# Kernel optimization log

Measured on AMD Instinct MI355X. Metric: run time of the kernel, lower is better.

The kernel has to match this reference:

```python
import jax, jax.numpy as jnp
import numpy as np

B, T, H, K = 128, 512, 1024, 7
START, STOP = 5, 6
NEG = -10000.0


def setup_inputs() -> dict:
    key = jax.random.key(0)
    k1, k2, k3, k4, k5, k6 = jax.random.split(key, 6)
    features = jax.random.normal(k1, (B, T, H), dtype=jnp.float32)
    tags = jax.random.randint(k2, (B, T), 0, 5, dtype=jnp.int32)  # BIESO only
    lengths = jax.random.randint(k3, (B,), 1, T + 1, dtype=jnp.int32)
    W = jax.random.normal(k4, (K, H), dtype=jnp.float32) * (1.0 / np.sqrt(H))
    b = jax.random.normal(k5, (K,), dtype=jnp.float32) * 0.01
    transitions = jax.random.normal(k6, (K, K), dtype=jnp.float32)
    transitions = transitions.at[START, :].set(NEG)  # nothing transitions into START
    transitions = transitions.at[:, STOP].set(NEG)   # nothing transitions out of STOP
    return {"features": features, "tags": tags, "lengths": lengths,
            "W": W, "b": b, "transitions": transitions}


def _crf_loss(features, W, b, transitions, tags, lengths):
    feats = jnp.einsum('bth,kh->btk', features, W) + b  # [B,T,K] emissions
    Bn, Tn, Kn = feats.shape

    # ---- forward algorithm (partition function) ----
    init = jnp.full((Bn, Kn), NEG, dtype=feats.dtype).at[:, START].set(0.0)

    def step(fv, inp):
        emit, i = inp  # emit: [B,K]
        # tag_var[b, next, prev] = emit[b, next] + trans[next, prev] + fv[b, prev]
        tv = emit[:, :, None] + transitions[None, :, :] + fv[:, None, :]
        new = jax.nn.logsumexp(tv, axis=2)  # [B,K]
        fv = jnp.where((i < lengths)[:, None], new, fv)  # freeze past sentence end
        return fv, None

    fv, _ = jax.lax.scan(step, init, (jnp.swapaxes(feats, 0, 1), jnp.arange(Tn)))
    terminal = fv + transitions[STOP][None, :]
    forward_score = jax.nn.logsumexp(terminal, axis=1)  # [B]

    # ---- gold score ----
    pad_start = jnp.concatenate(
        [jnp.full((Bn, 1), START, tags.dtype), tags], axis=1)  # [B,T+1]
    pad_stop = jnp.concatenate(
        [tags, jnp.full((Bn, 1), STOP, tags.dtype)], axis=1)   # [B,T+1]
    j = jnp.arange(Tn + 1)[None, :]
    pad_stop = jnp.where(j >= lengths[:, None], STOP, pad_stop)
    trans_sc = jnp.sum(
        jnp.where(j <= lengths[:, None], transitions[pad_stop, pad_start], 0.0),
        axis=1)
    t = jnp.arange(Tn)[None, :]
    emit_sel = jnp.take_along_axis(feats, tags[:, :, None].astype(jnp.int32), axis=2)[:, :, 0]
    emit_sc = jnp.sum(jnp.where(t < lengths[:, None], emit_sel, 0.0), axis=1)
    gold_score = trans_sc + emit_sc  # [B]

    return jnp.sum(forward_score - gold_score)


def reference(features, tags, lengths, W, b, transitions):
    return _crf_loss(features, W, b, transitions, tags, lengths)
```

## Files before the change

kernel.cpp:

```cpp
#include <hip/hip_runtime.h>

#define B_ 128
#define T_ 512
#define H_ 1024
#define K_ 7
#define START_ 5
#define STOP_ 6
#define LOG2E 1.4426950408889634f
#define LN2 0.6931471805599453f
#define NEG2 (-10000.0f * 1.4426950408889634f)
#define MS 57

__device__ __forceinline__ float fexp2(float x) { return __builtin_amdgcn_exp2f(x); }
__device__ __forceinline__ float flog2(float x) { return __builtin_amdgcn_logf(x); }

__global__ __launch_bounds__(256, 2) void emis_kernel(
    const float* __restrict__ features, const float* __restrict__ W,
    const float* __restrict__ bias, float* __restrict__ e2, float* __restrict__ out) {
  if (blockIdx.x == 0 && threadIdx.x == 0) out[0] = 0.0f;

  const int tid = threadIdx.x;
  const int lane = tid & 63;
  const int gwave = blockIdx.x * 4 + (tid >> 6);
  const int NW = 8192;

  float4 w[K_][4];
#pragma unroll
  for (int k = 0; k < K_; ++k)
#pragma unroll
    for (int c = 0; c < 4; ++c)
      w[k][c] = *(const float4*)(W + k * H_ + c * 256 + lane * 4);

  const int vidx = ((lane & 1) << 2) | (lane & 2) | ((lane >> 2) & 1);
  float myb = 0.0f;
  if (vidx < K_) myb = bias[vidx];

  float4 A0, A1, A2, A3, B0, B1, B2, B3;
  {
    const float4* fp = (const float4*)(features + (size_t)gwave * H_);
    A0 = fp[lane]; A1 = fp[64 + lane]; A2 = fp[128 + lane]; A3 = fp[192 + lane];
    const float4* gp = (const float4*)(features + (size_t)(gwave + NW) * H_);
    B0 = gp[lane]; B1 = gp[64 + lane]; B2 = gp[128 + lane]; B3 = gp[192 + lane];
  }

#pragma unroll
  for (int it = 0; it < 8; ++it) {
    const int cur = gwave + it * NW;
    float4 C0, C1, C2, C3;
    if (it < 6) {
      const float4* pp = (const float4*)(features + (size_t)(cur + 2 * NW) * H_);
      C0 = pp[lane]; C1 = pp[64 + lane]; C2 = pp[128 + lane]; C3 = pp[192 + lane];
    }

    float acc[8];
#pragma unroll
    for (int k = 0; k < 8; ++k) acc[k] = 0.0f;
#pragma unroll
    for (int k = 0; k < K_; ++k) {
      acc[k] += A0.x * w[k][0].x + A0.y * w[k][0].y + A0.z * w[k][0].z + A0.w * w[k][0].w;
      acc[k] += A1.x * w[k][1].x + A1.y * w[k][1].y + A1.z * w[k][1].z + A1.w * w[k][1].w;
      acc[k] += A2.x * w[k][2].x + A2.y * w[k][2].y + A2.z * w[k][2].z + A2.w * w[k][2].w;
      acc[k] += A3.x * w[k][3].x + A3.y * w[k][3].y + A3.z * w[k][3].z + A3.w * w[k][3].w;
    }

    const bool b0 = lane & 1;
    float k0 = b0 ? acc[4] : acc[0], s0 = b0 ? acc[0] : acc[4];
    float k1 = b0 ? acc[5] : acc[1], s1 = b0 ? acc[1] : acc[5];
    float k2 = b0 ? acc[6] : acc[2], s2 = b0 ? acc[2] : acc[6];
    float k3 = b0 ? acc[7] : acc[3], s3 = b0 ? acc[3] : acc[7];
    k0 += __shfl_xor(s0, 1, 64); k1 += __shfl_xor(s1, 1, 64);
    k2 += __shfl_xor(s2, 1, 64); k3 += __shfl_xor(s3, 1, 64);
    const bool b1 = lane & 2;
    float m0 = b1 ? k2 : k0, t0 = b1 ? k0 : k2;
    float m1 = b1 ? k3 : k1, t1 = b1 ? k1 : k3;
    m0 += __shfl_xor(t0, 2, 64); m1 += __shfl_xor(t1, 2, 64);
    const bool b2 = lane & 4;
    float x = b2 ? m1 : m0, y = b2 ? m0 : m1;
    x += __shfl_xor(y, 4, 64);
    x += __shfl_xor(x, 8, 64);
    x += __shfl_xor(x, 16, 64);
    x += __shfl_xor(x, 32, 64);

    if (lane < 8 && vidx < K_)
      e2[(size_t)cur * 8 + vidx] = (x + myb) * LOG2E;

    A0 = B0; A1 = B1; A2 = B2; A3 = B3;
    if (it < 6) { B0 = C0; B1 = C1; B2 = C2; B3 = C3; }
  }
}

template <int NM>
__device__ __forceinline__ void level_fn(const float* __restrict__ evenB,
                                         const float* __restrict__ oddB,
                                         int qstride, float* __restrict__ dst,
                                         int tid) {
  constexpr int TOT = NM * 49;
  constexpr int NI = (TOT + 255) / 256;
  float tmp[NI];
#pragma unroll
  for (int i = 0; i < NI; ++i) {
    const int u = tid + i * 256;
    if (u < TOT) {
      const int q = u / 49, r = u - 49 * q, n = r / 7, p = r - 7 * n;
      const float* hi = oddB + q * qstride;
      const float* lo = evenB + q * qstride;
      float qq[7];
#pragma unroll
      for (int m = 0; m < 7; ++m) qq[m] = hi[n * 8 + m] + lo[m * 8 + p];
      float mx = fmaxf(fmaxf(fmaxf(qq[0], qq[1]), fmaxf(qq[2], qq[3])),
                       fmaxf(fmaxf(qq[4], qq[5]), qq[6]));
      float s = 0.f;
#pragma unroll
      for (int m = 0; m < 7; ++m) s += fexp2(qq[m] - mx);
      tmp[i] = mx + flog2(s);
    }
  }
  __syncthreads();
#pragma unroll
  for (int i = 0; i < NI; ++i) {
    const int u = tid + i * 256;
    if (u < TOT) {
      const int q = u / 49, r = u - 49 * q, n = r / 7, p = r - 7 * n;
      dst[q * MS + n * 8 + p] = tmp[i];
    }
  }
  __syncthreads();
}

__global__ __launch_bounds__(256) void scan_kernel(
    const float* __restrict__ e2, const int* __restrict__ tags,
    const int* __restrict__ lengths, const float* __restrict__ transitions,
    float* __restrict__ out) {
  __shared__ float s0[128 * MS];
  __shared__ float s1[128 * MS];
  __shared__ float tr2s[49];
  __shared__ float red[4];

  const int tid = threadIdx.x;
  const int b = blockIdx.x;
  const int len = lengths[b];

  if (tid < 49) tr2s[tid] = transitions[tid] * LOG2E;
  __syncthreads();

  const int* tg = tags + (size_t)b * T_;
  const float* ep = e2 + (size_t)b * T_ * 8;
  float gp = 0.f;
  for (int t = tid; t < len; t += 256) {
    const int tag = tg[t];
    const int prev = t ? tg[t - 1] : START_;
    gp += ep[(size_t)t * 8 + tag] + tr2s[tag * 7 + prev];
  }
#pragma unroll
  for (int off = 32; off; off >>= 1) gp += __shfl_xor(gp, off, 64);
  if ((tid & 63) == 0) red[tid >> 6] = gp;

  {
    const int t0 = 2 * tid, t1 = 2 * tid + 1;
    float P[7][7];
    if (t1 < len) {
      const float* e0p = ep + (size_t)t0 * 8;
      float c[7], e1[7];
#pragma unroll
      for (int m = 0; m < 7; ++m) c[m] = e0p[m];
#pragma unroll
      for (int n = 0; n < 7; ++n) e1[n] = e0p[8 + n];
#pragma unroll
      for (int n = 0; n < 7; ++n) {
        float a[7];
#pragma unroll
        for (int m = 0; m < 7; ++m) a[m] = tr2s[n * 7 + m] + c[m];
#pragma unroll
        for (int p = 0; p < 7; ++p) {
          float q[7];
#pragma unroll
          for (int m = 0; m < 7; ++m) q[m] = a[m] + tr2s[m * 7 + p];
          float mx = fmaxf(fmaxf(fmaxf(q[0], q[1]), fmaxf(q[2], q[3])),
                           fmaxf(fmaxf(q[4], q[5]), q[6]));
          float s = 0.f;
#pragma unroll
          for (int m = 0; m < 7; ++m) s += fexp2(q[m] - mx);
          P[n][p] = e1[n] + mx + flog2(s);
        }
      }
    } else if (t0 < len) {
      const float* e0p = ep + (size_t)t0 * 8;
#pragma unroll
      for (int n = 0; n < 7; ++n) {
        const float e0n = e0p[n];
#pragma unroll
        for (int p = 0; p < 7; ++p) P[n][p] = e0n + tr2s[n * 7 + p];
      }
    } else {
#pragma unroll
      for (int n = 0; n < 7; ++n)
#pragma unroll
        for (int p = 0; p < 7; ++p) P[n][p] = (n == p) ? 0.f : NEG2;
    }
    float* dstm = ((tid & 1) ? s1 : s0) + (tid >> 1) * MS;
#pragma unroll
    for (int n = 0; n < 7; ++n)
#pragma unroll
      for (int p = 0; p < 7; ++p) dstm[n * 8 + p] = P[n][p];
  }
  __syncthreads();

  level_fn<128>(s0, s1, MS, s0, tid);
  level_fn<64>(s0, s0 + MS, 2 * MS, s1, tid);
  level_fn<32>(s1, s1 + MS, 2 * MS, s0, tid);
  level_fn<16>(s0, s0 + MS, 2 * MS, s1, tid);
  level_fn<8>(s1, s1 + MS, 2 * MS, s0, tid);
  level_fn<4>(s0, s0 + MS, 2 * MS, s1, tid);
  level_fn<2>(s1, s1 + MS, 2 * MS, s0, tid);
  level_fn<1>(s0, s0 + MS, 2 * MS, s1, tid);

  if (tid == 0) {
    float tt[7];
#pragma unroll
    for (int n = 0; n < 7; ++n) tt[n] = s1[n * 8 + START_] + tr2s[STOP_ * 7 + n];
    float mx = tt[0];
#pragma unroll
    for (int n = 1; n < 7; ++n) mx = fmaxf(mx, tt[n]);
    float s = 0.f;
#pragma unroll
    for (int n = 0; n < 7; ++n) s += fexp2(tt[n] - mx);
    const float fwd = mx + flog2(s);
    const float gold = red[0] + red[1] + red[2] + red[3] +
                       tr2s[STOP_ * 7 + tg[len - 1]];
    atomicAdd(out, (fwd - gold) * LN2);
  }
}

extern "C" void kernel_launch(void* const* d_in, const int* in_sizes, int n_in,
                              void* d_out, int out_size, void* d_ws, size_t ws_size,
                              hipStream_t stream) {
  const float* features    = (const float*)d_in[0];
  const int*   tags        = (const int*)d_in[1];
  const int*   lengths     = (const int*)d_in[2];
  const float* W           = (const float*)d_in[3];
  const float* bias        = (const float*)d_in[4];
  const float* transitions = (const float*)d_in[5];
  float* out = (float*)d_out;
  float* e2  = (float*)d_ws;

  emis_kernel<<<2048, 256, 0, stream>>>(features, W, bias, e2, out);
  scan_kernel<<<B_, 256, 0, stream>>>(e2, tags, lengths, transitions, out);
}
```

Baseline: 63.87 us.

## Deepen emission prefetch with nontemporal loads; widen scan block and drop max-shift

The emission kernel now keeps three rows in flight instead of two and reads features through nontemporal loads, aiming to hide more HBM latency on the streaming 256MB read. The scan kernel moves to 512 threads: half build the pairwise transfer matrices while the other half compute the gold score in parallel, and the tree-reduction levels spread over more threads. The leaf logsumexp drops its max subtraction and adds a tiny epsilon, trading numerical safety for fewer ops. The extra live registers in the emission kernel could lower occupancy, and skipping the max can underflow when all terms are very negative, since transitions contain -10000 entries.

```diff
diff --git a/kernel.cpp b/kernel.cpp
--- a/kernel.cpp
+++ b/kernel.cpp
@@ -11,8 +11,13 @@
 #define NEG2 (-10000.0f * 1.4426950408889634f)
 #define MS 57
 
+typedef float f32x4 __attribute__((ext_vector_type(4)));
+
 __device__ __forceinline__ float fexp2(float x) { return __builtin_amdgcn_exp2f(x); }
 __device__ __forceinline__ float flog2(float x) { return __builtin_amdgcn_logf(x); }
+__device__ __forceinline__ f32x4 ntload(const float* p) {
+  return __builtin_nontemporal_load((const f32x4*)p);
+}
 
 __global__ __launch_bounds__(256, 2) void emis_kernel(
     const float* __restrict__ features, const float* __restrict__ W,
@@ -24,32 +29,34 @@
   const int gwave = blockIdx.x * 4 + (tid >> 6);
   const int NW = 8192;
 
-  float4 w[K_][4];
+  f32x4 w[K_][4];
 #pragma unroll
   for (int k = 0; k < K_; ++k)
 #pragma unroll
     for (int c = 0; c < 4; ++c)
-      w[k][c] = *(const float4*)(W + k * H_ + c * 256 + lane * 4);
+      w[k][c] = *(const f32x4*)(W + k * H_ + c * 256 + lane * 4);
 
   const int vidx = ((lane & 1) << 2) | (lane & 2) | ((lane >> 2) & 1);
   float myb = 0.0f;
   if (vidx < K_) myb = bias[vidx];
 
-  float4 A0, A1, A2, A3, B0, B1, B2, B3;
+  f32x4 A0, A1, A2, A3, B0, B1, B2, B3, C0, C1, C2, C3;
   {
-    const float4* fp = (const float4*)(features + (size_t)gwave * H_);
-    A0 = fp[lane]; A1 = fp[64 + lane]; A2 = fp[128 + lane]; A3 = fp[192 + lane];
-    const float4* gp = (const float4*)(features + (size_t)(gwave + NW) * H_);
-    B0 = gp[lane]; B1 = gp[64 + lane]; B2 = gp[128 + lane]; B3 = gp[192 + lane];
+    const float* fp = features + (size_t)gwave * H_ + lane * 4;
+    A0 = ntload(fp); A1 = ntload(fp + 256); A2 = ntload(fp + 512); A3 = ntload(fp + 768);
+    const float* gp = fp + (size_t)NW * H_;
+    B0 = ntload(gp); B1 = ntload(gp + 256); B2 = ntload(gp + 512); B3 = ntload(gp + 768);
+    const float* hp = gp + (size_t)NW * H_;
+    C0 = ntload(hp); C1 = ntload(hp + 256); C2 = ntload(hp + 512); C3 = ntload(hp + 768);
   }
 
 #pragma unroll
   for (int it = 0; it < 8; ++it) {
     const int cur = gwave + it * NW;
-    float4 C0, C1, C2, C3;
-    if (it < 6) {
-      const float4* pp = (const float4*)(features + (size_t)(cur + 2 * NW) * H_);
-      C0 = pp[lane]; C1 = pp[64 + lane]; C2 = pp[128 + lane]; C3 = pp[192 + lane];
+    f32x4 D0, D1, D2, D3;
+    if (it < 5) {
+      const float* pp = features + (size_t)(cur + 3 * NW) * H_ + lane * 4;
+      D0 = ntload(pp); D1 = ntload(pp + 256); D2 = ntload(pp + 512); D3 = ntload(pp + 768);
     }
 
     float acc[8];
@@ -85,7 +92,8 @@
       e2[(size_t)cur * 8 + vidx] = (x + myb) * LOG2E;
 
     A0 = B0; A1 = B1; A2 = B2; A3 = B3;
-    if (it < 6) { B0 = C0; B1 = C1; B2 = C2; B3 = C3; }
+    B0 = C0; B1 = C1; B2 = C2; B3 = C3;
+    if (it < 5) { C0 = D0; C1 = D1; C2 = D2; C3 = D3; }
   }
 }
 
@@ -95,11 +103,11 @@
                                          int qstride, float* __restrict__ dst,
                                          int tid) {
   constexpr int TOT = NM * 49;
-  constexpr int NI = (TOT + 255) / 256;
+  constexpr int NI = (TOT + 511) / 512;
   float tmp[NI];
 #pragma unroll
   for (int i = 0; i < NI; ++i) {
-    const int u = tid + i * 256;
+    const int u = tid + i * 512;
     if (u < TOT) {
       const int q = u / 49, r = u - 49 * q, n = r / 7, p = r - 7 * n;
       const float* hi = oddB + q * qstride;
@@ -118,7 +126,7 @@
   __syncthreads();
 #pragma unroll
   for (int i = 0; i < NI; ++i) {
-    const int u = tid + i * 256;
+    const int u = tid + i * 512;
     if (u < TOT) {
       const int q = u / 49, r = u - 49 * q, n = r / 7, p = r - 7 * n;
       dst[q * MS + n * 8 + p] = tmp[i];
@@ -127,7 +135,7 @@
   __syncthreads();
 }
 
-__global__ __launch_bounds__(256) void scan_kernel(
+__global__ __launch_bounds__(512) void scan_kernel(
     const float* __restrict__ e2, const int* __restrict__ tags,
     const int* __restrict__ lengths, const float* __restrict__ transitions,
     float* __restrict__ out) {
@@ -145,17 +153,8 @@
 
   const int* tg = tags + (size_t)b * T_;
   const float* ep = e2 + (size_t)b * T_ * 8;
-  float gp = 0.f;
-  for (int t = tid; t < len; t += 256) {
-    const int tag = tg[t];
-    const int prev = t ? tg[t - 1] : START_;
-    gp += ep[(size_t)t * 8 + tag] + tr2s[tag * 7 + prev];
-  }
-#pragma unroll
-  for (int off = 32; off; off >>= 1) gp += __shfl_xor(gp, off, 64);
-  if ((tid & 63) == 0) red[tid >> 6] = gp;
-
-  {
+
+  if (tid < 256) {
     const int t0 = 2 * tid, t1 = 2 * tid + 1;
     float P[7][7];
     if (t1 < len) {
@@ -172,15 +171,10 @@
         for (int m = 0; m < 7; ++m) a[m] = tr2s[n * 7 + m] + c[m];
 #pragma unroll
         for (int p = 0; p < 7; ++p) {
-          float q[7];
-#pragma unroll
-          for (int m = 0; m < 7; ++m) q[m] = a[m] + tr2s[m * 7 + p];
-          float mx = fmaxf(fmaxf(fmaxf(q[0], q[1]), fmaxf(q[2], q[3])),
-                           fmaxf(fmaxf(q[4], q[5]), q[6]));
-          float s = 0.f;
-#pragma unroll
-          for (int m = 0; m < 7; ++m) s += fexp2(q[m] - mx);
-          P[n][p] = e1[n] + mx + flog2(s);
+          float s = 1e-37f;
+#pragma unroll
+          for (int m = 0; m < 7; ++m) s += fexp2(a[m] + tr2s[m * 7 + p]);
+          P[n][p] = e1[n] + flog2(s);
         }
       }
     } else if (t0 < len) {
@@ -202,6 +196,17 @@
     for (int n = 0; n < 7; ++n)
 #pragma unroll
       for (int p = 0; p < 7; ++p) dstm[n * 8 + p] = P[n][p];
+  } else {
+    const int t2 = tid - 256;
+    float gp = 0.f;
+    for (int t = t2; t < len; t += 256) {
+      const int tag = tg[t];
+      const int prev = t ? tg[t - 1] : START_;
+      gp += ep[(size_t)t * 8 + tag] + tr2s[tag * 7 + prev];
+    }
+#pragma unroll
+    for (int off = 32; off; off >>= 1) gp += __shfl_xor(gp, off, 64);
+    if ((tid & 63) == 0) red[(tid >> 6) - 4] = gp;
   }
   __syncthreads();
 
@@ -244,5 +249,5 @@
   float* e2  = (float*)d_ws;
 
   emis_kernel<<<2048, 256, 0, stream>>>(features, W, bias, e2, out);
-  scan_kernel<<<B_, 256, 0, stream>>>(e2, tags, lengths, transitions, out);
-}
+  scan_kernel<<<B_, 512, 0, stream>>>(e2, tags, lengths, transitions, out);
+}
```

After: 63.12 us. No clear change (-1.2%).
